# Kernel tuning notes

Hardware: AMD Instinct MI355X
Metric: run time of the kernel (lower is better)

Reference implementation:

```python
import jax, jax.numpy as jnp
import numpy as np

D = H = W = 64
N = D * H * W
BS = 2
C = 32          # enc_dim
IN_DIM = 4
OUT_DIM = 4
P = 5           # pos_enc_dim
COND = 32
M = 8           # modes per axis
NL = 4          # n_layers
NODE_IN = IN_DIM + 3 + 2 * P * 3   # 37
ENC_T = 1 + 2 * P                  # 11
ENC_C = ENC_T * COND               # 352
DT = 0.05


def fourier_embedding(pos, n_freq):
    # F(x) = [cos(2^i*pi*x_l), sin(2^i*pi*x_l)] per coordinate l, then concat x
    freq = (2.0 ** jnp.arange(n_freq, dtype=jnp.float32)) * jnp.pi  # (P,)
    ang = pos[..., None] * freq                                     # (..., L, P)
    emb = jnp.concatenate([jnp.cos(ang), jnp.sin(ang)], axis=-1)    # (..., L, 2P)
    emb = emb.reshape(*pos.shape[:-1], -1)                          # (..., L*2P)
    return jnp.concatenate([emb, pos], axis=-1)


def setup_inputs() -> dict:
    key = jax.random.key(0)
    ks = jax.random.split(key, 24)
    scale = 1.0 / C ** 2
    inp = {
        "state_in": jax.random.normal(ks[0], (BS, N, IN_DIM), jnp.float32),
        "node_pos": jax.random.uniform(ks[1], (BS, N, 3), jnp.float32),
        "edges": jax.random.randint(ks[2], (BS, 16, 2), 0, N),
        "time_i": jax.random.uniform(ks[3], (BS, 1), jnp.float32),
        "conditions": jax.random.uniform(ks[4], (BS, COND), jnp.float32),
        "t_embed_w": jax.random.normal(ks[5], (C, ENC_T), jnp.float32) * 0.05,
        "t_embed_b": jax.random.normal(ks[6], (C,), jnp.float32) * 0.05,
        "c_embed_w": jax.random.normal(ks[7], (C, ENC_C), jnp.float32) * 0.05,
        "c_embed_b": jax.random.normal(ks[8], (C,), jnp.float32) * 0.05,
        "lift_w": jax.random.normal(ks[9], (C, NODE_IN), jnp.float32) * 0.05,
        "lift_b": jax.random.normal(ks[10], (C,), jnp.float32) * 0.05,
        "spec_wr": jax.random.uniform(ks[11], (NL, C, C, M, M, M), jnp.float32) * scale,
        "spec_wi": jax.random.uniform(ks[12], (NL, C, C, M, M, M), jnp.float32) * scale,
        "byp_w": jax.random.normal(ks[13], (NL, C, C), jnp.float32) * 0.05,
        "byp_b": jax.random.normal(ks[14], (NL, C), jnp.float32) * 0.05,
        "proj1_w": jax.random.normal(ks[15], (C, C), jnp.float32) * 0.05,
        "proj1_b": jax.random.normal(ks[16], (C,), jnp.float32) * 0.05,
        "proj2_w": jax.random.normal(ks[17], (OUT_DIM, C), jnp.float32) * 0.05,
        "proj2_b": jax.random.normal(ks[18], (OUT_DIM,), jnp.float32) * 0.05,
    }
    return inp


def _conv1x1(x, w, b):
    # x: (b, c, d, h, w), w: (o, c), b: (o,)
    return jnp.einsum('bcdhw,oc->bodhw', x, w) + b[None, :, None, None, None]


def _fno_forward(state_in, node_pos, time_i, conditions,
                 t_embed_w, t_embed_b, c_embed_w, c_embed_b, lift_w, lift_b,
                 spec_wr, spec_wi, byp_w, byp_b, proj1_w, proj1_b, proj2_w, proj2_b):
    pos_enc = fourier_embedding(node_pos, P)      # (bs, N, 33)
    c_enc = fourier_embedding(conditions, P)      # (bs, 352)
    t_enc = fourier_embedding(time_i, P)          # (bs, 11)

    node_feat = jnp.concatenate([state_in, pos_enc], axis=-1)  # (bs, N, 37)
    t_emb = (t_enc @ t_embed_w.T + t_embed_b)[:, :, None, None, None]
    c_emb = (c_enc @ c_embed_w.T + c_embed_b)[:, :, None, None, None]

    # (bs, N, 37) -> (bs, 37, D, H, W)
    x = node_feat.transpose(0, 2, 1).reshape(BS, NODE_IN, D, H, W)
    x = _conv1x1(x, lift_w, lift_b)
    x = x + t_emb + c_emb

    for l in range(NL):
        w = jax.lax.complex(spec_wr[l], spec_wi[l])              # (C, C, M, M, M)
        x_ft = jnp.fft.rfftn(x, axes=(-3, -2, -1))               # (bs, C, D, H, W//2+1)
        blk = jnp.einsum('bixyz,ioxyz->boxyz', x_ft[..., :M, :M, :M], w)
        out_ft = jnp.zeros_like(x_ft).at[..., :M, :M, :M].set(blk)
        sp = jnp.fft.irfftn(out_ft, s=(D, H, W), axes=(-3, -2, -1))
        bp = _conv1x1(x, byp_w[l], byp_b[l])
        x = jax.nn.gelu(sp + bp, approximate=False)

    x = jax.nn.gelu(_conv1x1(x, proj1_w, proj1_b), approximate=False)
    x = _conv1x1(x, proj2_w, proj2_b)                            # (bs, 4, D, H, W)
    v_pred = x.reshape(BS, OUT_DIM, N).transpose(0, 2, 1)        # (bs, N, 4)
    return state_in + DT * v_pred


def reference(state_in, node_pos, edges, time_i, conditions,
              t_embed_w, t_embed_b, c_embed_w, c_embed_b, lift_w, lift_b,
              spec_wr, spec_wi, byp_w, byp_b, proj1_w, proj1_b, proj2_w, proj2_b):
    # edges are unused in the FNO forward (kept for API compatibility)
    return _fno_forward(state_in, node_pos, time_i, conditions,
                        t_embed_w, t_embed_b, c_embed_w, c_embed_b, lift_w, lift_b,
                        spec_wr, spec_wi, byp_w, byp_b, proj1_w, proj1_b, proj2_w, proj2_b)
```

## Files before the change

kernel.cpp:

```cpp
#include <hip/hip_runtime.h>
#include <math.h>

#define PI_F 3.14159265358979323846f

typedef __bf16 bf16x8 __attribute__((ext_vector_type(8)));
typedef float floatx4 __attribute__((ext_vector_type(4)));
union U8 { unsigned short u[8]; uint4 q; bf16x8 v; };

__device__ __forceinline__ float gelu_sig(float v) {
    float e = __builtin_amdgcn_exp2f(-2.4554670f * v);
    return v * __builtin_amdgcn_rcpf(1.0f + e);
}
__device__ __forceinline__ int rfl(int x) { return __builtin_amdgcn_readfirstlane(x); }

__device__ __forceinline__ unsigned short f2bf(float f) {
    unsigned int u = __float_as_uint(f);
    u += 0x7fffu + ((u >> 16) & 1u);
    return (unsigned short)(u >> 16);
}
__device__ __forceinline__ float bf2f(unsigned short h) {
    return __uint_as_float(((unsigned int)h) << 16);
}
__device__ __forceinline__ unsigned int pack2(float a, float b) {
    return (unsigned int)f2bf(a) | ((unsigned int)f2bf(b) << 16);
}
__device__ __forceinline__ uint2 pack4h(unsigned short a, unsigned short b,
                                        unsigned short c, unsigned short d) {
    return make_uint2((unsigned int)a | ((unsigned int)b << 16),
                      (unsigned int)c | ((unsigned int)d << 16));
}

__global__ void k_wt(const float* __restrict__ time_i, const float* __restrict__ conditions,
                     const float* __restrict__ t_embed_w, const float* __restrict__ t_embed_b,
                     const float* __restrict__ c_embed_w, const float* __restrict__ c_embed_b,
                     const float* __restrict__ lift_b, float* __restrict__ embk,
                     const float* __restrict__ byp_w, const float* __restrict__ lift_w,
                     unsigned short* __restrict__ wbh, unsigned short* __restrict__ wlbf,
                     unsigned short* __restrict__ Tinv, unsigned short* __restrict__ TfT,
                     float* __restrict__ Tp1g) {
    const float th = PI_F / 32.0f;
    int t = threadIdx.x;
    if (blockIdx.x < 2) {
        __shared__ float red[8][32];
        int b = blockIdx.x;
        int c = t & 31, lg = t >> 5;
        float acc = 0.0f;
        if (lg == 0) {
            acc = t_embed_b[c] + c_embed_b[c] + lift_b[c];
            float tv = time_i[b];
            float ang = PI_F * tv;
            const float* tw = t_embed_w + c * 11;
            for (int i = 0; i < 5; i++) {
                float s, co; sincosf(ang, &s, &co);
                acc += co * tw[i] + s * tw[5 + i];
                ang *= 2.0f;
            }
            acc += tv * tw[10];
        }
        const float* cw = c_embed_w + c * 352;
        for (int j = 0; j < 4; j++) {
            int l = lg * 4 + j;
            float v = conditions[b * 32 + l];
            float ang = PI_F * v;
            for (int i = 0; i < 5; i++) {
                float s, co; sincosf(ang, &s, &co);
                acc += co * cw[l * 10 + i] + s * cw[l * 10 + 5 + i];
                ang *= 2.0f;
            }
            acc += v * cw[320 + l];
        }
        red[lg][c] = acc;
        __syncthreads();
        if (t < 32) {
            float s = 0.0f;
            for (int g = 0; g < 8; g++) s += red[g][t];
            embk[b * 32 + t] = s;
        }
        return;
    }
    int idx = (blockIdx.x - 2) * 256 + t;
    if (idx < 4096) {
        wbh[idx] = f2bf(byp_w[idx]);
    } else if (idx < 6144) {
        int j = idx - 4096;
        int o = j >> 6, q = j & 63;
        wlbf[j] = (q < 37) ? f2bf(lift_w[o * 37 + q]) : 0;
    } else if (idx < 8192) {
        int j = idx - 6144;
        int nz = j >> 5, k = j & 31;
        int kz = k >> 1;
        float val = 0.0f;
        if (kz < 8) {
            float a = (float)((kz * nz) & 63) * th;
            val = (k & 1) ? sinf(a) : cosf(a);
            val *= (kz == 0) ? (1.0f / 262144.0f) : (2.0f / 262144.0f);
        }
        Tinv[j] = f2bf(val);
    } else if (idx < 9216) {
        int j = idx - 8192;
        int kcol = j >> 6, nz = j & 63;
        int kz = kcol >> 1;
        float a = (float)((kz * nz) & 63) * th;
        float val = (kcol & 1) ? -sinf(a) : cosf(a);
        TfT[j] = f2bf(val);
    } else if (idx < 9728) {
        int j = idx - 9216;
        int ny = j >> 3, ky = j & 7;
        float a = (float)((ky * ny) & 63) * th;
        Tp1g[j * 2] = cosf(a);
        Tp1g[j * 2 + 1] = sinf(a);
    }
}

__device__ __forceinline__ void swz8k(int blk, int& b, int& nx, int& ny) {
    int x = blk & 7;
    int j = blk >> 3;
    int pair = x * 16 + (j >> 6);
    ny = j & 63;
    b = pair >> 6;
    nx = pair & 63;
}

__global__ __launch_bounds__(256) void k_lift(const float* __restrict__ state_in,
        const float* __restrict__ node_pos, const unsigned short* __restrict__ wlbf,
        const float* __restrict__ embk, const unsigned short* __restrict__ TfT,
        unsigned short* __restrict__ x0, unsigned int* __restrict__ a1) {
    __shared__ __align__(16) float SL[3488];
    unsigned short* fsT  = (unsigned short*)SL;
    unsigned short* ysbf = (unsigned short*)(SL + 2304);
    float* bias = SL + 3456;
    int t = threadIdx.x;
    int b, nx, ny; swz8k(blockIdx.x, b, nx, ny);
    int nxy = nx * 64 + ny;

    if (t < 32) bias[t] = embk[b * 32 + t];
    {
        for (int u = t; u < 2048; u += 256) {
            int row = u >> 5, col = 37 + (u & 31);
            fsT[row * 72 + col] = 0;
        }
    }
    if (t < 192) {
        int nzf = t / 3;
        int l = t - nzf * 3;
        float p = node_pos[((size_t)b * 262144 + (nxy << 6)) * 3 + t];
        float s, c; sincosf(PI_F * p, &s, &c);
        unsigned short* row = fsT + nzf * 72;
        #pragma unroll
        for (int i = 0; i < 5; i++) {
            row[4 + l * 10 + i] = f2bf(c);
            row[4 + l * 10 + 5 + i] = f2bf(s);
            float nc = 2.0f * c * c - 1.0f;
            s = 2.0f * s * c;
            c = nc;
        }
        row[34 + l] = f2bf(p);
    } else {
        int nzf = t - 192;
        const float4 s4 = *(const float4*)(state_in + ((size_t)b * 262144 + (nxy << 6) + nzf) * 4);
        unsigned short* row = fsT + nzf * 72;
        row[0] = f2bf(s4.x); row[1] = f2bf(s4.y);
        row[2] = f2bf(s4.z); row[3] = f2bf(s4.w);
    }
    __syncthreads();

    int lane = t & 63;
    int w = rfl(t >> 6);
    int l15 = lane & 15;
    int quad = lane >> 4;
    int nz = w * 16 + l15;
    size_t xbase = ((size_t)(b * 4096 + nxy)) * 2048;

    U8 b0, b1_;
    b0.q  = *(const uint4*)(fsT + nz * 72 + (quad << 3));
    b1_.q = *(const uint4*)(fsT + nz * 72 + 32 + (quad << 3));
    #pragma unroll
    for (int ot = 0; ot < 2; ot++) {
        U8 aA, aB;
        aA.q = *(const uint4*)(wlbf + ((ot * 16 + l15) << 6) + (quad << 3));
        aB.q = *(const uint4*)(wlbf + ((ot * 16 + l15) << 6) + 32 + (quad << 3));
        floatx4 cb;
        #pragma unroll
        for (int r = 0; r < 4; r++) cb[r] = bias[ot * 16 + quad * 4 + r];
        floatx4 d = __builtin_amdgcn_mfma_f32_16x16x32_bf16(aA.v, b0.v, cb, 0, 0, 0);
        d = __builtin_amdgcn_mfma_f32_16x16x32_bf16(aB.v, b1_.v, d, 0, 0, 0);
        unsigned short h[4];
        #pragma unroll
        for (int r = 0; r < 4; r++) {
            h[r] = f2bf(d[r]);
            ysbf[(ot * 16 + quad * 4 + r) * 72 + nz] = h[r];
        }
        *(uint2*)(x0 + xbase + nz * 32 + ot * 16 + (quad << 2)) =
            pack4h(h[0], h[1], h[2], h[3]);
    }
    __syncthreads();

    if (w < 2) {
        int o = w * 16 + l15;
        U8 ay0, ay1, bt0, bt1;
        ay0.q = *(const uint4*)(ysbf + o * 72 + (quad << 3));
        ay1.q = *(const uint4*)(ysbf + o * 72 + 32 + (quad << 3));
        bt0.q = *(const uint4*)(TfT + (l15 << 6) + (quad << 3));
        bt1.q = *(const uint4*)(TfT + (l15 << 6) + 32 + (quad << 3));
        floatx4 z = {0.0f, 0.0f, 0.0f, 0.0f};
        z = __builtin_amdgcn_mfma_f32_16x16x32_bf16(ay0.v, bt0.v, z, 0, 0, 0);
        z = __builtin_amdgcn_mfma_f32_16x16x32_bf16(ay1.v, bt1.v, z, 0, 0, 0);
        float p0 = __shfl_xor(z[0], 1), p1 = __shfl_xor(z[1], 1);
        float p2 = __shfl_xor(z[2], 1), p3 = __shfl_xor(z[3], 1);
        if (!(lane & 1)) {
            unsigned int* a1p = a1 + ((size_t)(b * 4096 + nxy)) * 256;
            int kz = l15 >> 1;
            a1p[(w * 16 + quad * 4 + 0) * 8 + kz] = pack2(z[0], p0);
            a1p[(w * 16 + quad * 4 + 1) * 8 + kz] = pack2(z[1], p1);
            a1p[(w * 16 + quad * 4 + 2) * 8 + kz] = pack2(z[2], p2);
            a1p[(w * 16 + quad * 4 + 3) * 8 + kz] = pack2(z[3], p3);
        }
    }
}


__global__ __launch_bounds__(256) void k_p1(const unsigned int* __restrict__ a1,
        const float2* __restrict__ Tp1g, float2* __restrict__ a2p) {
    int blk = blockIdx.x, t = threadIdx.x;
    int x = blk & 7, r = blk >> 3;
    int pair = x * 16 + (r & 15);
    int qtr = r >> 4;
    const unsigned int* src = a1 + ((size_t)(pair * 64 + qtr * 16)) * 256 + t;
    float accr[8], acci[8];
    #pragma unroll
    for (int k = 0; k < 8; k++) { accr[k] = 0.0f; acci[k] = 0.0f; }
    #pragma unroll 4
    for (int j = 0; j < 16; j++) {
        int ny = qtr * 16 + j;
        unsigned int pv = src[(size_t)j * 256];
        float vx = bf2f((unsigned short)(pv & 0xffffu));
        float vy = bf2f((unsigned short)(pv >> 16));
        const float2* tw = Tp1g + ny * 8;
        #pragma unroll
        for (int ky = 0; ky < 8; ky++) {
            float2 w2 = tw[ky];
            accr[ky] += vx * w2.x + vy * w2.y;
            acci[ky] += vy * w2.x - vx * w2.y;
        }
    }
    float4* dst = (float4*)(a2p + (size_t)qtr * 262144 + ((size_t)(pair * 256 + t)) * 8);
    #pragma unroll
    for (int j = 0; j < 4; j++)
        dst[j] = make_float4(accr[2 * j], acci[2 * j], accr[2 * j + 1], acci[2 * j + 1]);
}

__global__ __launch_bounds__(256) void k_p2(const float2* __restrict__ a2p,
                                            float2* __restrict__ xft) {
    __shared__ __align__(16) float2 SH[1040];
    int blk = blockIdx.x, t = threadIdx.x;
    for (int lu = 0; lu < 2; lu++) {
        int un = blk * 2 + lu;
        int b = un >> 8, ckz = un & 255;
        size_t base = (size_t)b * 131072 + (size_t)ckz * 8;
        for (int e = t; e < 512; e += 256) {
            size_t a = base + (size_t)(e >> 3) * 2048 + (e & 7);
            float2 v0 = a2p[a];
            float2 v1 = a2p[a + 262144];
            float2 v2 = a2p[a + 524288];
            float2 v3 = a2p[a + 786432];
            SH[lu * 520 + e] = make_float2(v0.x + v1.x + v2.x + v3.x,
                                           v0.y + v1.y + v2.y + v3.y);
        }
    }
    __syncthreads();
    if (t < 128) {
        int lu = t >> 6, out = t & 63;
        int un = blk * 2 + lu;
        int kx = out & 7;
        float sn, cc; sincosf((float)kx * (PI_F / 32.0f), &sn, &cc);
        float bsn = -sn;
        float tc = 1.0f, ts = 0.0f, rr = 0.0f, ri = 0.0f;
        const float2* row = SH + lu * 520 + (out >> 3);
        for (int nx = 0; nx < 64; nx++) {
            float2 v = row[nx * 8];
            rr += v.x * tc - v.y * ts;
            ri += v.x * ts + v.y * tc;
            float nt = tc * cc - ts * bsn; ts = ts * cc + tc * bsn; tc = nt;
        }
        xft[(size_t)un * 64 + out] = make_float2(rr, ri);
    }
}

__global__ __launch_bounds__(256) void k_p3(const float2* __restrict__ xft,
        const float* __restrict__ wr, const float* __restrict__ wi,
        float2* __restrict__ yftp) {
    __shared__ __align__(16) float2 SH[64];
    int blk = blockIdx.x, t = threadIdx.x;
    int unit = blk >> 2, iq = blk & 3;
    int b = unit >> 6, kx = (unit >> 3) & 7, ky = unit & 7;
    if (t < 64) {
        int il = t >> 3, kz = t & 7;
        int i = iq * 8 + il;
        SH[t] = xft[((size_t)((b * 32 + i) * 8 + kz)) * 64 + ky * 8 + kx];
    }
    __syncthreads();
    int o = t >> 3, kz = t & 7;
    float yr = 0.0f, yi = 0.0f;
    for (int il = 0; il < 8; il++) {
        int i = iq * 8 + il;
        float2 xv = SH[il * 8 + kz];
        int wofs = ((i * 32 + o) << 9) + kx * 64 + ky * 8 + kz;
        float wrv = wr[wofs], wiv = wi[wofs];
        yr += xv.x * wrv - xv.y * wiv;
        yi += xv.x * wiv + xv.y * wrv;
    }
    yftp[(size_t)iq * 32768 + ((size_t)((b * 32 + o) * 8 + kz)) * 64 + ky * 8 + kx]
        = make_float2(yr, yi);
}

__global__ __launch_bounds__(256) void k_p4(const float2* __restrict__ yftp,
                                            float2* __restrict__ b1) {
    __shared__ __align__(16) float2 SH[4608];
    int blk = blockIdx.x, t = threadIdx.x;
    for (int u = 0; u < 2; u++) {
        if (u) __syncthreads();
        int unit = blk * 2 + u;
        int b = unit >> 8, nx = (unit >> 2) & 63, og = unit & 3;
        size_t sbase = ((size_t)(b * 32 + og * 8)) * 512;
        for (int e = t; e < 4096; e += 256) {
            float2 v0 = yftp[sbase + e];
            float2 v1 = yftp[32768 + sbase + e];
            float2 v2 = yftp[65536 + sbase + e];
            float2 v3 = yftp[98304 + sbase + e];
            SH[(e >> 3) * 9 + (e & 7)] = make_float2(v0.x + v1.x + v2.x + v3.x,
                                                     v0.y + v1.y + v2.y + v3.y);
        }
        __syncthreads();
        float cs, ss; sincosf((float)nx * (PI_F / 32.0f), &ss, &cs);
        float2* dst = b1 + ((size_t)(b * 64 + nx)) * 2048 + og * 512;
        for (int h = 0; h < 2; h++) {
            int idx = h * 256 + t;
            const float2* row = SH + idx * 9;
            float c = 1.0f, s = 0.0f, rr = 0.0f, ri = 0.0f;
            #pragma unroll
            for (int kx = 0; kx < 8; kx++) {
                float2 y = row[kx];
                rr += y.x * c - y.y * s;
                ri += y.x * s + y.y * c;
                float nc = c * cs - s * ss; s = s * cs + c * ss; c = nc;
            }
            dst[idx] = make_float2(rr, ri);
        }
    }
}

__global__ __launch_bounds__(256) void k_fin(
        const unsigned short* __restrict__ xin, const float2* __restrict__ b1,
        const unsigned short* __restrict__ wbh, const float* __restrict__ bb,
        const unsigned short* __restrict__ Tinv, const unsigned short* __restrict__ TfT,
        const float2* __restrict__ Tp1g, unsigned short* __restrict__ xout,
        unsigned int* __restrict__ a1, int do_z, int do_proj,
        const float* __restrict__ state_in, const float* __restrict__ p1w,
        const float* __restrict__ p1b, const float* __restrict__ p2w,
        const float* __restrict__ p2b, float* __restrict__ outp) {
    __shared__ __align__(16) float S[2848];
    float* pr = S;
    unsigned short* msbf = (unsigned short*)(S + 1024);
    unsigned short* ysbf = (unsigned short*)(S + 1664);
    float* bias = S + 2816;
    int t = threadIdx.x;
    int b, nx, ny; swz8k(blockIdx.x, b, nx, ny);
    int nxy = nx * 64 + ny;
    int lane = t & 63;
    int w = rfl(t >> 6);
    int l15 = lane & 15;
    int quad = lane >> 4;
    int nz = w * 16 + l15;
    size_t xbase = ((size_t)(b * 4096 + nxy)) * 2048;

    U8 bx, btv, aw0, aw1;
    bx.q  = *(const uint4*)(xin + xbase + nz * 32 + (quad << 3));
    btv.q = *(const uint4*)(Tinv + (nz << 5) + (quad << 3));
    aw0.q = *(const uint4*)(wbh + (l15 << 5) + (quad << 3));
    aw1.q = *(const uint4*)(wbh + ((16 + l15) << 5) + (quad << 3));

    if (t >= 96 && t < 128) bias[t - 96] = bb[t - 96];
    ((unsigned int*)msbf)[(t >> 3) * 20 + 8 + (t & 7)] = 0;
    {
        const float4* g = (const float4*)(b1 + ((size_t)(b * 64 + nx)) * 2048
                                          + (size_t)t * 8);
        float4 g0 = g[0], g1 = g[1], g2 = g[2], g3 = g[3];
        float vr[8], vi[8];
        vr[0] = g0.x; vi[0] = g0.y; vr[1] = g0.z; vi[1] = g0.w;
        vr[2] = g1.x; vi[2] = g1.y; vr[3] = g1.z; vi[3] = g1.w;
        vr[4] = g2.x; vi[4] = g2.y; vr[5] = g2.z; vi[5] = g2.w;
        vr[6] = g3.x; vi[6] = g3.y; vr[7] = g3.z; vi[7] = g3.w;
        const float2* tw = Tp1g + ny * 8;
        float mr = 0.0f, mi = 0.0f;
        #pragma unroll
        for (int ky = 0; ky < 8; ky++) {
            float2 w2 = tw[ky];
            mr += vr[ky] * w2.x - vi[ky] * w2.y;
            mi += vr[ky] * w2.y + vi[ky] * w2.x;
        }
        ((unsigned int*)msbf)[(t >> 3) * 20 + (t & 7)] = pack2(mr, -mi);
    }
    __syncthreads();

    U8 am0, am1;
    am0.q = *(const uint4*)(msbf + l15 * 40 + (quad << 3));
    am1.q = *(const uint4*)(msbf + (16 + l15) * 40 + (quad << 3));
    floatx4 cb0, cb1;
    #pragma unroll
    for (int r = 0; r < 4; r++) {
        cb0[r] = bias[quad * 4 + r];
        cb1[r] = bias[16 + quad * 4 + r];
    }
    floatx4 d0 = __builtin_amdgcn_mfma_f32_16x16x32_bf16(aw0.v, bx.v, cb0, 0, 0, 0);
    d0 = __builtin_amdgcn_mfma_f32_16x16x32_bf16(am0.v, btv.v, d0, 0, 0, 0);
    floatx4 d1 = __builtin_amdgcn_mfma_f32_16x16x32_bf16(aw1.v, bx.v, cb1, 0, 0, 0);
    d1 = __builtin_amdgcn_mfma_f32_16x16x32_bf16(am1.v, btv.v, d1, 0, 0, 0);

    unsigned short h0[4], h1[4];
    #pragma unroll
    for (int r = 0; r < 4; r++) {
        h0[r] = f2bf(gelu_sig(d0[r]));
        ysbf[(quad * 4 + r) * 72 + nz] = h0[r];
        h1[r] = f2bf(gelu_sig(d1[r]));
        ysbf[(16 + quad * 4 + r) * 72 + nz] = h1[r];
    }
    if (!do_proj) {
        *(uint2*)(xout + xbase + nz * 32 + (quad << 2)) =
            pack4h(h0[0], h0[1], h0[2], h0[3]);
        *(uint2*)(xout + xbase + nz * 32 + 16 + (quad << 2)) =
            pack4h(h1[0], h1[1], h1[2], h1[3]);
    }
    __syncthreads();

    if (do_z && w < 2) {
        int o = w * 16 + l15;
        U8 ay0, ay1, bt0, bt1;
        ay0.q = *(const uint4*)(ysbf + o * 72 + (quad << 3));
        ay1.q = *(const uint4*)(ysbf + o * 72 + 32 + (quad << 3));
        bt0.q = *(const uint4*)(TfT + (l15 << 6) + (quad << 3));
        bt1.q = *(const uint4*)(TfT + (l15 << 6) + 32 + (quad << 3));
        floatx4 z = {0.0f, 0.0f, 0.0f, 0.0f};
        z = __builtin_amdgcn_mfma_f32_16x16x32_bf16(ay0.v, bt0.v, z, 0, 0, 0);
        z = __builtin_amdgcn_mfma_f32_16x16x32_bf16(ay1.v, bt1.v, z, 0, 0, 0);
        float p0 = __shfl_xor(z[0], 1), p1 = __shfl_xor(z[1], 1);
        float p2 = __shfl_xor(z[2], 1), p3 = __shfl_xor(z[3], 1);
        if (!(lane & 1)) {
            unsigned int* a1p = a1 + ((size_t)(b * 4096 + nxy)) * 256;
            int kz = l15 >> 1;
            a1p[(w * 16 + quad * 4 + 0) * 8 + kz] = pack2(z[0], p0);
            a1p[(w * 16 + quad * 4 + 1) * 8 + kz] = pack2(z[1], p1);
            a1p[(w * 16 + quad * 4 + 2) * 8 + kz] = pack2(z[2], p2);
            a1p[(w * 16 + quad * 4 + 3) * 8 + kz] = pack2(z[3], p3);
        }
    }

    if (do_proj) {
        int nzp = t & 63;
        float xv[32];
        #pragma unroll
        for (int i = 0; i < 32; i++) xv[i] = bf2f(ysbf[i * 72 + nzp]);
        float r0 = 0.f, r1 = 0.f, r2 = 0.f, r3 = 0.f;
        #pragma unroll
        for (int k = 0; k < 8; k++) {
            int o = w * 8 + k;
            float a = p1b[o];
            const float* wr = p1w + o * 32;
            #pragma unroll
            for (int i = 0; i < 32; i++) a += wr[i] * xv[i];
            float h = gelu_sig(a);
            r0 += p2w[0 * 32 + o] * h;
            r1 += p2w[1 * 32 + o] * h;
            r2 += p2w[2 * 32 + o] * h;
            r3 += p2w[3 * 32 + o] * h;
        }
        *(float4*)(pr + w * 256 + nzp * 4) = make_float4(r0, r1, r2, r3);
        __syncthreads();
        if (t < 64) {
            float4 a0 = *(float4*)(pr + 0 * 256 + t * 4);
            float4 a1_ = *(float4*)(pr + 1 * 256 + t * 4);
            float4 a2 = *(float4*)(pr + 2 * 256 + t * 4);
            float4 a3 = *(float4*)(pr + 3 * 256 + t * 4);
            size_t base = ((size_t)b * 262144 + (nxy << 6) + t) * 4;
            float4 sv = *(const float4*)(state_in + base);
            *(float4*)(outp + base) = make_float4(
                sv.x + 0.05f * (p2b[0] + a0.x + a1_.x + a2.x + a3.x),
                sv.y + 0.05f * (p2b[1] + a0.y + a1_.y + a2.y + a3.y),
                sv.z + 0.05f * (p2b[2] + a0.z + a1_.z + a2.z + a3.z),
                sv.w + 0.05f * (p2b[3] + a0.w + a1_.w + a2.w + a3.w));
        }
    }
}

extern "C" void kernel_launch(void* const* d_in, const int* in_sizes, int n_in,
                              void* d_out, int out_size, void* d_ws, size_t ws_size,
                              hipStream_t stream) {
    const float* state_in   = (const float*)d_in[0];
    const float* node_pos   = (const float*)d_in[1];
    const float* time_i     = (const float*)d_in[3];
    const float* conditions = (const float*)d_in[4];
    const float* t_embed_w  = (const float*)d_in[5];
    const float* t_embed_b  = (const float*)d_in[6];
    const float* c_embed_w  = (const float*)d_in[7];
    const float* c_embed_b  = (const float*)d_in[8];
    const float* lift_w     = (const float*)d_in[9];
    const float* lift_b     = (const float*)d_in[10];
    const float* spec_wr    = (const float*)d_in[11];
    const float* spec_wi    = (const float*)d_in[12];
    const float* byp_w      = (const float*)d_in[13];
    const float* byp_b      = (const float*)d_in[14];
    const float* proj1_w    = (const float*)d_in[15];
    const float* proj1_b    = (const float*)d_in[16];
    const float* proj2_w    = (const float*)d_in[17];
    const float* proj2_b    = (const float*)d_in[18];
    float* out = (float*)d_out;
    float* ws  = (float*)d_ws;

    unsigned short* xA = (unsigned short*)ws;
    unsigned short* xB = (unsigned short*)(ws + 8388608);
    unsigned int* a1 = (unsigned int*)(ws + 16777216);
    float2* a2p  = (float2*)(ws + 20971520);
    float2* xft  = (float2*)(ws + 23068672);
    float2* yftp = (float2*)(ws + 23134208);
    float2* b1   = (float2*)(ws + 23396352);
    float*  embk = ws + 23920640;
    unsigned short* wbh  = (unsigned short*)(ws + 23920704);
    unsigned short* wlbf = (unsigned short*)(ws + 23922752);
    unsigned short* Tinv = (unsigned short*)(ws + 23923776);
    unsigned short* TfT  = (unsigned short*)(ws + 23924800);
    float* Tp1gf = ws + 23925312;
    float2* Tp1g = (float2*)Tp1gf;

    k_wt<<<40, 256, 0, stream>>>(time_i, conditions, t_embed_w, t_embed_b,
                                 c_embed_w, c_embed_b, lift_b, embk,
                                 byp_w, lift_w, wbh, wlbf, Tinv, TfT, Tp1gf);
    k_lift<<<8192, 256, 0, stream>>>(state_in, node_pos, wlbf, embk, TfT, xA, a1);

    for (int l = 0; l < 4; l++) {
        unsigned short* xin  = (l & 1) ? xB : xA;
        unsigned short* xout = (l & 1) ? xA : xB;
        const float* wrl = spec_wr + (size_t)l * 524288;
        const float* wil = spec_wi + (size_t)l * 524288;
        k_p1<<<512, 256, 0, stream>>>(a1, Tp1g, a2p);
        k_p2<<<256, 256, 0, stream>>>(a2p, xft);
        k_p3<<<512, 256, 0, stream>>>(xft, wrl, wil, yftp);
        k_p4<<<256, 256, 0, stream>>>(yftp, b1);
        k_fin<<<8192, 256, 0, stream>>>(xin, b1, wbh + l * 1024, byp_b + l * 32,
                                        Tinv, TfT, Tp1g, xout, a1, (l < 3) ? 1 : 0,
                                        (l == 3) ? 1 : 0, state_in,
                                        proj1_w, proj1_b, proj2_w, proj2_b, out);
    }
}
```

Baseline: 351.7 us.

## Fuse spectral x-DFT, channel mixing and inverse x-DFT into one kernel per layer

Replaces the four small spectral-stage kernels (x-axis DFT, per-mode channel mix, partial reduction, inverse x-DFT) with a single kernel per (batch, kz, ky) mode block. The spectral weights are pre-transposed once into a complex interleaved mode-major layout inside the setup kernel. This cuts launches and round trips through intermediate buffers on every layer. It also changes the x-tensor channel layout so lift and fin write 16-byte stores instead of two 8-byte stores, and reorganises the a2p and b1 layouts to suit the fused kernel. In exchange the fused kernel runs on only 128 blocks, which may leave much of the GPU idle, and the setup kernel gains a large weight-transpose pass.

```diff
diff --git a/kernel.cpp b/kernel.cpp
--- a/kernel.cpp
+++ b/kernel.cpp
@@ -23,11 +23,6 @@
 }
 __device__ __forceinline__ unsigned int pack2(float a, float b) {
     return (unsigned int)f2bf(a) | ((unsigned int)f2bf(b) << 16);
-}
-__device__ __forceinline__ uint2 pack4h(unsigned short a, unsigned short b,
-                                        unsigned short c, unsigned short d) {
-    return make_uint2((unsigned int)a | ((unsigned int)b << 16),
-                      (unsigned int)c | ((unsigned int)d << 16));
 }
 
 __global__ void k_wt(const float* __restrict__ time_i, const float* __restrict__ conditions,
@@ -37,11 +32,13 @@
                      const float* __restrict__ byp_w, const float* __restrict__ lift_w,
                      unsigned short* __restrict__ wbh, unsigned short* __restrict__ wlbf,
                      unsigned short* __restrict__ Tinv, unsigned short* __restrict__ TfT,
-                     float* __restrict__ Tp1g) {
+                     float* __restrict__ Tp1g, const float* __restrict__ spec_wr,
+                     const float* __restrict__ spec_wi, float2* __restrict__ wT) {
     const float th = PI_F / 32.0f;
+    __shared__ float red[8][32];
+    __shared__ __align__(16) float2 TT[4160];
     int t = threadIdx.x;
     if (blockIdx.x < 2) {
-        __shared__ float red[8][32];
         int b = blockIdx.x;
         int c = t & 31, lg = t >> 5;
         float acc = 0.0f;
@@ -75,6 +72,25 @@
             float s = 0.0f;
             for (int g = 0; g < 8; g++) s += red[g][t];
             embk[b * 32 + t] = s;
+        }
+        return;
+    }
+    if (blockIdx.x >= 40) {
+        int n = blockIdx.x - 40;
+        int l = n >> 7, i = (n & 127) >> 2, og = n & 3;
+        size_t srcb = ((size_t)(l * 1024 + i * 32 + og * 8)) * 512;
+        for (int k = 0; k < 16; k++) {
+            int e = k * 256 + t;
+            TT[(e >> 9) * 520 + (e & 511)] =
+                make_float2(spec_wr[srcb + e], spec_wi[srcb + e]);
+        }
+        __syncthreads();
+        for (int k = 0; k < 16; k++) {
+            int e = k * 256 + t;
+            int o = e & 7, mo = e >> 3;
+            int sm = ((mo & 7) << 6) | (mo & 56) | (mo >> 6);
+            wT[(size_t)l * 524288 + (size_t)mo * 1024 + i * 32 + og * 8 + o]
+                = TT[o * 520 + sm];
         }
         return;
     }
@@ -121,6 +137,7 @@
     nx = pair & 63;
 }
 
+
 __global__ __launch_bounds__(256) void k_lift(const float* __restrict__ state_in,
         const float* __restrict__ node_pos, const unsigned short* __restrict__ wlbf,
         const float* __restrict__ embk, const unsigned short* __restrict__ TfT,
@@ -174,6 +191,7 @@
     U8 b0, b1_;
     b0.q  = *(const uint4*)(fsT + nz * 72 + (quad << 3));
     b1_.q = *(const uint4*)(fsT + nz * 72 + 32 + (quad << 3));
+    unsigned short hh[2][4];
     #pragma unroll
     for (int ot = 0; ot < 2; ot++) {
         U8 aA, aB;
@@ -184,15 +202,17 @@
         for (int r = 0; r < 4; r++) cb[r] = bias[ot * 16 + quad * 4 + r];
         floatx4 d = __builtin_amdgcn_mfma_f32_16x16x32_bf16(aA.v, b0.v, cb, 0, 0, 0);
         d = __builtin_amdgcn_mfma_f32_16x16x32_bf16(aB.v, b1_.v, d, 0, 0, 0);
-        unsigned short h[4];
         #pragma unroll
         for (int r = 0; r < 4; r++) {
-            h[r] = f2bf(d[r]);
-            ysbf[(ot * 16 + quad * 4 + r) * 72 + nz] = h[r];
-        }
-        *(uint2*)(x0 + xbase + nz * 32 + ot * 16 + (quad << 2)) =
-            pack4h(h[0], h[1], h[2], h[3]);
-    }
+            hh[ot][r] = f2bf(d[r]);
+            ysbf[(ot * 16 + quad * 4 + r) * 72 + nz] = hh[ot][r];
+        }
+    }
+    *(uint4*)(x0 + xbase + nz * 32 + (quad << 3)) = make_uint4(
+        (unsigned)hh[0][0] | ((unsigned)hh[0][1] << 16),
+        (unsigned)hh[0][2] | ((unsigned)hh[0][3] << 16),
+        (unsigned)hh[1][0] | ((unsigned)hh[1][1] << 16),
+        (unsigned)hh[1][2] | ((unsigned)hh[1][3] << 16));
     __syncthreads();
 
     if (w < 2) {
@@ -219,7 +239,7 @@
 }
 
 
-__global__ __launch_bounds__(256) void k_p1(const unsigned int* __restrict__ a1,
+__global__ __launch_bounds__(256) void k_ps1(const unsigned int* __restrict__ a1,
         const float2* __restrict__ Tp1g, float2* __restrict__ a2p) {
     int blk = blockIdx.x, t = threadIdx.x;
     int x = blk & 7, r = blk >> 3;
@@ -243,108 +263,76 @@
             acci[ky] += vy * w2.x - vx * w2.y;
         }
     }
-    float4* dst = (float4*)(a2p + (size_t)qtr * 262144 + ((size_t)(pair * 256 + t)) * 8);
+    int b = pair >> 6, nx = pair & 63;
+    int c = t >> 3, kz = t & 7;
+    float2* dst = a2p + ((size_t)((qtr * 2 + b) * 8 + kz)) * 16384 + nx * 32 + c;
     #pragma unroll
-    for (int j = 0; j < 4; j++)
-        dst[j] = make_float4(accr[2 * j], acci[2 * j], accr[2 * j + 1], acci[2 * j + 1]);
-}
-
-__global__ __launch_bounds__(256) void k_p2(const float2* __restrict__ a2p,
-                                            float2* __restrict__ xft) {
-    __shared__ __align__(16) float2 SH[1040];
-    int blk = blockIdx.x, t = threadIdx.x;
-    for (int lu = 0; lu < 2; lu++) {
-        int un = blk * 2 + lu;
-        int b = un >> 8, ckz = un & 255;
-        size_t base = (size_t)b * 131072 + (size_t)ckz * 8;
-        for (int e = t; e < 512; e += 256) {
-            size_t a = base + (size_t)(e >> 3) * 2048 + (e & 7);
-            float2 v0 = a2p[a];
-            float2 v1 = a2p[a + 262144];
-            float2 v2 = a2p[a + 524288];
-            float2 v3 = a2p[a + 786432];
-            SH[lu * 520 + e] = make_float2(v0.x + v1.x + v2.x + v3.x,
-                                           v0.y + v1.y + v2.y + v3.y);
-        }
-    }
-    __syncthreads();
-    if (t < 128) {
-        int lu = t >> 6, out = t & 63;
-        int un = blk * 2 + lu;
-        int kx = out & 7;
+    for (int ky = 0; ky < 8; ky++)
+        dst[(size_t)ky * 2048] = make_float2(accr[ky], acci[ky]);
+}
+
+__global__ __launch_bounds__(256) void k_ps2(const float2* __restrict__ a2p,
+        const float2* __restrict__ wTl, const float2* __restrict__ Tp1g,
+        float2* __restrict__ b1) {
+    __shared__ __align__(16) float2 MS[2048];
+    __shared__ __align__(16) float2 XS[256];
+    __shared__ __align__(16) float2 YS[288];
+    int t = threadIdx.x, blk = blockIdx.x;
+    int b = blk >> 6, kz = (blk >> 3) & 7, ky = blk & 7;
+    size_t sb = (size_t)b * 131072 + kz * 16384 + ky * 2048;
+    for (int k = 0; k < 8; k++) {
+        int e = k * 256 + t;
+        float2 v0 = a2p[sb + e];
+        float2 v1 = a2p[sb + 262144 + e];
+        float2 v2 = a2p[sb + 524288 + e];
+        float2 v3 = a2p[sb + 786432 + e];
+        MS[e] = make_float2(v0.x + v1.x + v2.x + v3.x,
+                            v0.y + v1.y + v2.y + v3.y);
+    }
+    __syncthreads();
+    {
+        int c = t >> 3, kx = t & 7;
         float sn, cc; sincosf((float)kx * (PI_F / 32.0f), &sn, &cc);
         float bsn = -sn;
-        float tc = 1.0f, ts = 0.0f, rr = 0.0f, ri = 0.0f;
-        const float2* row = SH + lu * 520 + (out >> 3);
+        float tc = 1.0f, ts = 0.0f, xr = 0.0f, xi = 0.0f;
         for (int nx = 0; nx < 64; nx++) {
-            float2 v = row[nx * 8];
-            rr += v.x * tc - v.y * ts;
-            ri += v.x * ts + v.y * tc;
+            float2 v = MS[nx * 32 + c];
+            xr += v.x * tc - v.y * ts;
+            xi += v.x * ts + v.y * tc;
             float nt = tc * cc - ts * bsn; ts = ts * cc + tc * bsn; tc = nt;
         }
-        xft[(size_t)un * 64 + out] = make_float2(rr, ri);
-    }
-}
-
-__global__ __launch_bounds__(256) void k_p3(const float2* __restrict__ xft,
-        const float* __restrict__ wr, const float* __restrict__ wi,
-        float2* __restrict__ yftp) {
-    __shared__ __align__(16) float2 SH[64];
-    int blk = blockIdx.x, t = threadIdx.x;
-    int unit = blk >> 2, iq = blk & 3;
-    int b = unit >> 6, kx = (unit >> 3) & 7, ky = unit & 7;
-    if (t < 64) {
-        int il = t >> 3, kz = t & 7;
-        int i = iq * 8 + il;
-        SH[t] = xft[((size_t)((b * 32 + i) * 8 + kz)) * 64 + ky * 8 + kx];
-    }
-    __syncthreads();
-    int o = t >> 3, kz = t & 7;
-    float yr = 0.0f, yi = 0.0f;
-    for (int il = 0; il < 8; il++) {
-        int i = iq * 8 + il;
-        float2 xv = SH[il * 8 + kz];
-        int wofs = ((i * 32 + o) << 9) + kx * 64 + ky * 8 + kz;
-        float wrv = wr[wofs], wiv = wi[wofs];
-        yr += xv.x * wrv - xv.y * wiv;
-        yi += xv.x * wiv + xv.y * wrv;
-    }
-    yftp[(size_t)iq * 32768 + ((size_t)((b * 32 + o) * 8 + kz)) * 64 + ky * 8 + kx]
-        = make_float2(yr, yi);
-}
-
-__global__ __launch_bounds__(256) void k_p4(const float2* __restrict__ yftp,
-                                            float2* __restrict__ b1) {
-    __shared__ __align__(16) float2 SH[4608];
-    int blk = blockIdx.x, t = threadIdx.x;
-    for (int u = 0; u < 2; u++) {
-        if (u) __syncthreads();
-        int unit = blk * 2 + u;
-        int b = unit >> 8, nx = (unit >> 2) & 63, og = unit & 3;
-        size_t sbase = ((size_t)(b * 32 + og * 8)) * 512;
-        for (int e = t; e < 4096; e += 256) {
-            float2 v0 = yftp[sbase + e];
-            float2 v1 = yftp[32768 + sbase + e];
-            float2 v2 = yftp[65536 + sbase + e];
-            float2 v3 = yftp[98304 + sbase + e];
-            SH[(e >> 3) * 9 + (e & 7)] = make_float2(v0.x + v1.x + v2.x + v3.x,
-                                                     v0.y + v1.y + v2.y + v3.y);
-        }
-        __syncthreads();
-        float cs, ss; sincosf((float)nx * (PI_F / 32.0f), &ss, &cs);
-        float2* dst = b1 + ((size_t)(b * 64 + nx)) * 2048 + og * 512;
-        for (int h = 0; h < 2; h++) {
-            int idx = h * 256 + t;
-            const float2* row = SH + idx * 9;
-            float c = 1.0f, s = 0.0f, rr = 0.0f, ri = 0.0f;
+        XS[c * 8 + kx] = make_float2(xr, xi);
+    }
+    __syncthreads();
+    {
+        int kx = t >> 5, o = t & 31;
+        const float2* wp = wTl + ((size_t)(kz * 64 + ky * 8 + kx)) * 1024 + o;
+        float yr = 0.0f, yi = 0.0f;
+        #pragma unroll 8
+        for (int i = 0; i < 32; i++) {
+            float2 xv = XS[i * 8 + kx];
+            float2 wv = wp[i * 32];
+            yr += xv.x * wv.x - xv.y * wv.y;
+            yi += xv.x * wv.y + xv.y * wv.x;
+        }
+        YS[o * 9 + kx] = make_float2(yr, yi);
+    }
+    __syncthreads();
+    {
+        int nx8 = t >> 5, o = t & 31;
+        for (int j = 0; j < 8; j++) {
+            int nx = nx8 * 8 + j;
+            const float2* tw = Tp1g + nx * 8;
+            float rr = 0.0f, ri = 0.0f;
             #pragma unroll
             for (int kx = 0; kx < 8; kx++) {
-                float2 y = row[kx];
-                rr += y.x * c - y.y * s;
-                ri += y.x * s + y.y * c;
-                float nc = c * cs - s * ss; s = s * cs + c * ss; c = nc;
+                float2 y = YS[o * 9 + kx];
+                float2 w2 = tw[kx];
+                rr += y.x * w2.x - y.y * w2.y;
+                ri += y.x * w2.y + y.y * w2.x;
             }
-            dst[idx] = make_float2(rr, ri);
+            b1[((size_t)(b * 64 + nx)) * 2048 + (kz * 8 + ky) * 32 + o]
+                = make_float2(rr, ri);
         }
     }
 }
@@ -373,8 +361,11 @@
     int nz = w * 16 + l15;
     size_t xbase = ((size_t)(b * 4096 + nxy)) * 2048;
 
+    int posA = ((quad & 1) << 4) | ((quad >> 1) << 2);
+    uint2 xlo = *(const uint2*)(xin + xbase + nz * 32 + posA);
+    uint2 xhi = *(const uint2*)(xin + xbase + nz * 32 + posA + 8);
     U8 bx, btv, aw0, aw1;
-    bx.q  = *(const uint4*)(xin + xbase + nz * 32 + (quad << 3));
+    ((uint2*)&bx)[0] = xlo; ((uint2*)&bx)[1] = xhi;
     btv.q = *(const uint4*)(Tinv + (nz << 5) + (quad << 3));
     aw0.q = *(const uint4*)(wbh + (l15 << 5) + (quad << 3));
     aw1.q = *(const uint4*)(wbh + ((16 + l15) << 5) + (quad << 3));
@@ -382,21 +373,16 @@
     if (t >= 96 && t < 128) bias[t - 96] = bb[t - 96];
     ((unsigned int*)msbf)[(t >> 3) * 20 + 8 + (t & 7)] = 0;
     {
-        const float4* g = (const float4*)(b1 + ((size_t)(b * 64 + nx)) * 2048
-                                          + (size_t)t * 8);
-        float4 g0 = g[0], g1 = g[1], g2 = g[2], g3 = g[3];
-        float vr[8], vi[8];
-        vr[0] = g0.x; vi[0] = g0.y; vr[1] = g0.z; vi[1] = g0.w;
-        vr[2] = g1.x; vi[2] = g1.y; vr[3] = g1.z; vi[3] = g1.w;
-        vr[4] = g2.x; vi[4] = g2.y; vr[5] = g2.z; vi[5] = g2.w;
-        vr[6] = g3.x; vi[6] = g3.y; vr[7] = g3.z; vi[7] = g3.w;
+        const float2* g = b1 + ((size_t)(b * 64 + nx)) * 2048
+                          + (size_t)((t & 7) * 256 + (t >> 3));
         const float2* tw = Tp1g + ny * 8;
         float mr = 0.0f, mi = 0.0f;
         #pragma unroll
         for (int ky = 0; ky < 8; ky++) {
+            float2 v = g[ky * 32];
             float2 w2 = tw[ky];
-            mr += vr[ky] * w2.x - vi[ky] * w2.y;
-            mi += vr[ky] * w2.y + vi[ky] * w2.x;
+            mr += v.x * w2.x - v.y * w2.y;
+            mi += v.x * w2.y + v.y * w2.x;
         }
         ((unsigned int*)msbf)[(t >> 3) * 20 + (t & 7)] = pack2(mr, -mi);
     }
@@ -425,10 +411,11 @@
         ysbf[(16 + quad * 4 + r) * 72 + nz] = h1[r];
     }
     if (!do_proj) {
-        *(uint2*)(xout + xbase + nz * 32 + (quad << 2)) =
-            pack4h(h0[0], h0[1], h0[2], h0[3]);
-        *(uint2*)(xout + xbase + nz * 32 + 16 + (quad << 2)) =
-            pack4h(h1[0], h1[1], h1[2], h1[3]);
+        *(uint4*)(xout + xbase + nz * 32 + (quad << 3)) = make_uint4(
+            (unsigned)h0[0] | ((unsigned)h0[1] << 16),
+            (unsigned)h0[2] | ((unsigned)h0[3] << 16),
+            (unsigned)h1[0] | ((unsigned)h1[1] << 16),
+            (unsigned)h1[2] | ((unsigned)h1[3] << 16));
     }
     __syncthreads();
 
@@ -519,8 +506,6 @@
     unsigned short* xB = (unsigned short*)(ws + 8388608);
     unsigned int* a1 = (unsigned int*)(ws + 16777216);
     float2* a2p  = (float2*)(ws + 20971520);
-    float2* xft  = (float2*)(ws + 23068672);
-    float2* yftp = (float2*)(ws + 23134208);
     float2* b1   = (float2*)(ws + 23396352);
     float*  embk = ws + 23920640;
     unsigned short* wbh  = (unsigned short*)(ws + 23920704);
@@ -529,21 +514,19 @@
     unsigned short* TfT  = (unsigned short*)(ws + 23924800);
     float* Tp1gf = ws + 23925312;
     float2* Tp1g = (float2*)Tp1gf;
-
-    k_wt<<<40, 256, 0, stream>>>(time_i, conditions, t_embed_w, t_embed_b,
-                                 c_embed_w, c_embed_b, lift_b, embk,
-                                 byp_w, lift_w, wbh, wlbf, Tinv, TfT, Tp1gf);
+    float2* wT   = (float2*)(ws + 23926336);
+
+    k_wt<<<552, 256, 0, stream>>>(time_i, conditions, t_embed_w, t_embed_b,
+                                  c_embed_w, c_embed_b, lift_b, embk,
+                                  byp_w, lift_w, wbh, wlbf, Tinv, TfT, Tp1gf,
+                                  spec_wr, spec_wi, wT);
     k_lift<<<8192, 256, 0, stream>>>(state_in, node_pos, wlbf, embk, TfT, xA, a1);
 
     for (int l = 0; l < 4; l++) {
         unsigned short* xin  = (l & 1) ? xB : xA;
         unsigned short* xout = (l & 1) ? xA : xB;
-        const float* wrl = spec_wr + (size_t)l * 524288;
-        const float* wil = spec_wi + (size_t)l * 524288;
-        k_p1<<<512, 256, 0, stream>>>(a1, Tp1g, a2p);
-        k_p2<<<256, 256, 0, stream>>>(a2p, xft);
-        k_p3<<<512, 256, 0, stream>>>(xft, wrl, wil, yftp);
-        k_p4<<<256, 256, 0, stream>>>(yftp, b1);
+        k_ps1<<<512, 256, 0, stream>>>(a1, Tp1g, a2p);
+        k_ps2<<<128, 256, 0, stream>>>(a2p, wT + (size_t)l * 524288, Tp1g, b1);
         k_fin<<<8192, 256, 0, stream>>>(xin, b1, wbh + l * 1024, byp_b + l * 32,
                                         Tinv, TfT, Tp1g, xout, a1, (l < 3) ? 1 : 0,
                                         (l == 3) ? 1 : 0, state_in,
```

New measurement: 385.0 us. 9.5% more time.
